# Performance work log

Hardware: AMD Instinct MI355X
Metric: run time of the kernel (lower is better)

Reference implementation:

```python
import jax, jax.numpy as jnp
import numpy as np

N_NODES = 100000
N_EDGES = 640000
D = 128
EPS = 1e-5

def _full_layer_norm(x):
    # torch layer_norm with normalized_shape == x.shape: stats over ALL elements
    mu = jnp.mean(x)
    var = jnp.mean(jnp.square(x - mu))  # biased variance
    return (x - mu) * jax.lax.rsqrt(var + EPS)

def setup_inputs() -> dict:
    key = jax.random.key(0)
    k1, k2, k3, k4, k5 = jax.random.split(key, 5)
    scale1 = 1.0 / np.sqrt(D)
    scale2 = 1.0 / np.sqrt(2 * D)
    return {
        "edge_features": jax.random.normal(k1, (N_EDGES, D), dtype=jnp.float32),
        "node_features": jax.random.normal(k2, (N_NODES, D), dtype=jnp.float32),
        "edge_indices": jax.random.randint(k3, (N_EDGES, 2), 0, N_NODES, dtype=jnp.int32),
        "W1": jax.random.normal(k4, (D, D), dtype=jnp.float32) * scale1,
        "b1": jnp.zeros((D,), dtype=jnp.float32),
        "W2": jax.random.normal(k5, (2 * D, D), dtype=jnp.float32) * scale2,
        "b2": jnp.zeros((D,), dtype=jnp.float32),
    }

def reference(edge_features, node_features, edge_indices, W1, b1, W2, b2):
    # node MLP: linear -> whole-tensor layernorm -> gelu
    h = node_features @ W1 + b1                       # [N, D]
    h = jax.nn.gelu(_full_layer_norm(h), approximate=False)
    # gather source-node features onto edges
    src = edge_indices[:, 0]
    dst = edge_indices[:, 1]
    gathered = h[src]                                 # [E, D]
    e = jnp.concatenate([edge_features, gathered], axis=1)  # [E, 2D]
    e = e @ W2 + b2                                   # [E, D]
    e = jax.nn.gelu(_full_layer_norm(e), approximate=False)
    # scatter-mean (include_self=False): nodes with no in-edges stay 0
    seg_sum = jax.ops.segment_sum(e, dst, num_segments=N_NODES)       # [N, D]
    counts = jax.ops.segment_sum(jnp.ones((e.shape[0],), e.dtype), dst,
                                 num_segments=N_NODES)                 # [N]
    counts = counts[:, None]
    return jnp.where(counts > 0, seg_sum / jnp.maximum(counts, 1.0), 0.0)
```

## Files before the change

kernel.cpp:

```cpp
#include <hip/hip_runtime.h>
#include <hip/hip_bf16.h>
#include <math.h>

typedef __bf16 bf16;
typedef bf16 bf16x8 __attribute__((ext_vector_type(8)));
typedef float f32x4 __attribute__((ext_vector_type(4)));
typedef unsigned short ushort_t;

#define N_NODES 100000
#define N_EDGES 640000
#define DD 128
#define MAXDEG 64

__device__ __forceinline__ float gelu_f(float x) {
    return 0.5f * x * (1.0f + erff(x * 0.70710678118654752440f));
}

__device__ __forceinline__ float gelu_fast(float x) {
    float z2 = x * (1.595769122f + 0.071354816f * x * x);
    return x * __builtin_amdgcn_rcpf(1.0f + __expf(-z2));
}

__device__ __forceinline__ ushort_t bf16_bits(float x) {
    bf16 h = (bf16)x;
    return __builtin_bit_cast(ushort_t, h);
}

__device__ __forceinline__ float bits_to_f(ushort_t u) {
    return __uint_as_float(((unsigned)u) << 16);
}

#define K1_TILES 1563
__global__ __launch_bounds__(256) void k1_gemm1(
    const float* __restrict__ nf, const float* __restrict__ W1,
    const float* __restrict__ b1, ushort_t* __restrict__ hpre,
    float* __restrict__ psum, float* __restrict__ psq, int nblocks)
{
    __shared__ bf16 Ash[64 * 136];
    __shared__ float red[256];
    const int tid = threadIdx.x;
    const int lane = tid & 63;
    const int w = tid >> 6;
    const int l15 = lane & 15, l4 = lane >> 4;

    bf16x8 bfrag[4][2];
    #pragma unroll
    for (int s = 0; s < 4; ++s)
        #pragma unroll
        for (int t = 0; t < 2; ++t) {
            int n = w * 32 + t * 16 + l15;
            #pragma unroll
            for (int j = 0; j < 8; ++j)
                bfrag[s][t][j] = (bf16)W1[(s * 32 + l4 * 8 + j) * DD + n];
        }
    float bias[2];
    bias[0] = b1[w * 32 + l15];
    bias[1] = b1[w * 32 + 16 + l15];

    float lsum = 0.f, lsq = 0.f;
    const int srow = tid >> 2;
    const int q = tid & 3;

    for (int tile = blockIdx.x; tile < K1_TILES; tile += nblocks) {
        const int rbase = tile * 64;
        {
            int grow = min(rbase + srow, N_NODES - 1);
            const float4* p = (const float4*)&nf[(size_t)grow * DD + q * 32];
            #pragma unroll
            for (int u = 0; u < 4; ++u) {
                float4 a = p[2 * u], b = p[2 * u + 1];
                ushort_t o[8] = {bf16_bits(a.x), bf16_bits(a.y), bf16_bits(a.z), bf16_bits(a.w),
                                 bf16_bits(b.x), bf16_bits(b.y), bf16_bits(b.z), bf16_bits(b.w)};
                *(uint4*)&Ash[srow * 136 + q * 32 + u * 8] = *(const uint4*)o;
            }
        }
        __syncthreads();
        f32x4 acc[4][2];
        #pragma unroll
        for (int r = 0; r < 4; ++r)
            #pragma unroll
            for (int t = 0; t < 2; ++t)
                acc[r][t] = (f32x4){0.f, 0.f, 0.f, 0.f};
        #pragma unroll
        for (int s = 0; s < 4; ++s)
            #pragma unroll
            for (int r = 0; r < 4; ++r) {
                bf16x8 a = *(const bf16x8*)&Ash[(r * 16 + l15) * 136 + s * 32 + l4 * 8];
                acc[r][0] = __builtin_amdgcn_mfma_f32_16x16x32_bf16(a, bfrag[s][0], acc[r][0], 0, 0, 0);
                acc[r][1] = __builtin_amdgcn_mfma_f32_16x16x32_bf16(a, bfrag[s][1], acc[r][1], 0, 0, 0);
            }
        __syncthreads();
        #pragma unroll
        for (int r = 0; r < 4; ++r)
            #pragma unroll
            for (int t = 0; t < 2; ++t) {
                int n = w * 32 + t * 16 + l15;
                #pragma unroll
                for (int j = 0; j < 4; ++j) {
                    int rr = rbase + r * 16 + l4 * 4 + j;
                    if (rr < N_NODES) {
                        float v = acc[r][t][j] + bias[t];
                        hpre[(size_t)rr * DD + n] = bf16_bits(v);
                        lsum += v; lsq += v * v;
                    }
                }
            }
    }
    red[tid] = lsum; __syncthreads();
    for (int s = 128; s > 0; s >>= 1) { if (tid < s) red[tid] += red[tid + s]; __syncthreads(); }
    if (tid == 0) psum[blockIdx.x] = red[0];
    __syncthreads();
    red[tid] = lsq; __syncthreads();
    for (int s = 128; s > 0; s >>= 1) { if (tid < s) red[tid] += red[tid + s]; __syncthreads(); }
    if (tid == 0) psq[blockIdx.x] = red[0];
}

__global__ void k_reduce(const float* __restrict__ psum, const float* __restrict__ psq,
                         int nb, double cntd, float* __restrict__ scal)
{
    __shared__ double rs_[256], rq_[256];
    int tid = threadIdx.x;
    double s = 0.0, q = 0.0;
    for (int i = tid; i < nb; i += 256) { s += psum[i]; q += psq[i]; }
    rs_[tid] = s; rq_[tid] = q; __syncthreads();
    for (int st = 128; st > 0; st >>= 1) {
        if (tid < st) { rs_[tid] += rs_[tid + st]; rq_[tid] += rq_[tid + st]; }
        __syncthreads();
    }
    if (tid == 0) {
        double mu = rs_[0] / cntd;
        double var = rq_[0] / cntd - mu * mu;
        scal[0] = (float)mu;
        scal[1] = (float)(1.0 / sqrt(var + 1e-5));
    }
}

__global__ __launch_bounds__(256) void k3_act(
    const ushort_t* __restrict__ hpre, const float* __restrict__ scal,
    ushort_t* __restrict__ hg)
{
    const float mu = scal[0], rs = scal[1];
    size_t i = (size_t)(blockIdx.x * 256 + threadIdx.x) * 8;
    uint4 v = *(const uint4*)(hpre + i);
    const ushort_t* in = (const ushort_t*)&v;
    ushort_t o[8];
    #pragma unroll
    for (int j = 0; j < 8; ++j)
        o[j] = bf16_bits(gelu_f((bits_to_f(in[j]) - mu) * rs));
    *(uint4*)(hg + i) = *(const uint4*)o;
}

__global__ __launch_bounds__(256) void k4_gemm2(
    const float* __restrict__ ef, const ushort_t* __restrict__ hg,
    const int* __restrict__ eidx, const float* __restrict__ W2,
    const float* __restrict__ b2, ushort_t* __restrict__ e0,
    float* __restrict__ psum, float* __restrict__ psq, int nblocks)
{
    __shared__ bf16 Ash[64 * 264];
    __shared__ float red[256];
    const int tid = threadIdx.x;
    const int lane = tid & 63;
    const int w = tid >> 6;
    const int l15 = lane & 15, l4 = lane >> 4;

    bf16x8 bfrag[8][2];
    #pragma unroll
    for (int s = 0; s < 8; ++s)
        #pragma unroll
        for (int t = 0; t < 2; ++t) {
            int n = w * 32 + t * 16 + l15;
            #pragma unroll
            for (int j = 0; j < 8; ++j)
                bfrag[s][t][j] = (bf16)W2[(s * 32 + l4 * 8 + j) * DD + n];
        }
    float bias[2];
    bias[0] = b2[w * 32 + l15];
    bias[1] = b2[w * 32 + 16 + l15];

    float lsum = 0.f, lsq = 0.f;
    const int srow = tid >> 2;
    const int q = tid & 3;

    for (int tile = blockIdx.x; tile < N_EDGES / 64; tile += nblocks) {
        const int ebase = tile * 64;
        {
            const float4* p = (const float4*)&ef[(size_t)(ebase + srow) * DD + q * 32];
            #pragma unroll
            for (int u = 0; u < 4; ++u) {
                float4 a = p[2 * u], b = p[2 * u + 1];
                ushort_t o[8] = {bf16_bits(a.x), bf16_bits(a.y), bf16_bits(a.z), bf16_bits(a.w),
                                 bf16_bits(b.x), bf16_bits(b.y), bf16_bits(b.z), bf16_bits(b.w)};
                *(uint4*)&Ash[srow * 264 + q * 32 + u * 8] = *(const uint4*)o;
            }
            int src = eidx[(size_t)(ebase + srow) * 2];
            const uint4* hp = (const uint4*)&hg[(size_t)src * DD + q * 32];
            uint4* hd = (uint4*)&Ash[srow * 264 + 128 + q * 32];
            #pragma unroll
            for (int u = 0; u < 4; ++u) hd[u] = hp[u];
        }
        __syncthreads();
        f32x4 acc[4][2];
        #pragma unroll
        for (int r = 0; r < 4; ++r)
            #pragma unroll
            for (int t = 0; t < 2; ++t)
                acc[r][t] = (f32x4){0.f, 0.f, 0.f, 0.f};
        #pragma unroll
        for (int s = 0; s < 8; ++s)
            #pragma unroll
            for (int r = 0; r < 4; ++r) {
                bf16x8 a = *(const bf16x8*)&Ash[(r * 16 + l15) * 264 + s * 32 + l4 * 8];
                acc[r][0] = __builtin_amdgcn_mfma_f32_16x16x32_bf16(a, bfrag[s][0], acc[r][0], 0, 0, 0);
                acc[r][1] = __builtin_amdgcn_mfma_f32_16x16x32_bf16(a, bfrag[s][1], acc[r][1], 0, 0, 0);
            }
        __syncthreads();
        #pragma unroll
        for (int r = 0; r < 4; ++r)
            #pragma unroll
            for (int t = 0; t < 2; ++t) {
                int n = w * 32 + t * 16 + l15;
                #pragma unroll
                for (int j = 0; j < 4; ++j) {
                    float v = acc[r][t][j] + bias[t];
                    lsum += v; lsq += v * v;
                    int rr = ebase + r * 16 + l4 * 4 + j;
                    e0[(size_t)rr * DD + n] = bf16_bits(v);
                }
            }
    }
    red[tid] = lsum; __syncthreads();
    for (int s = 128; s > 0; s >>= 1) { if (tid < s) red[tid] += red[tid + s]; __syncthreads(); }
    if (tid == 0) psum[blockIdx.x] = red[0];
    __syncthreads();
    red[tid] = lsq; __syncthreads();
    for (int s = 128; s > 0; s >>= 1) { if (tid < s) red[tid] += red[tid + s]; __syncthreads(); }
    if (tid == 0) psq[blockIdx.x] = red[0];
}

__global__ __launch_bounds__(256) void k7_fill(
    const int* __restrict__ eidx, int* __restrict__ cnt, int* __restrict__ slot)
{
    int e = blockIdx.x * 256 + threadIdx.x;
    if (e >= N_EDGES) return;
    int dst = eidx[(size_t)e * 2 + 1];
    int pos = atomicAdd(&cnt[dst], 1);
    if (pos < MAXDEG) slot[dst * MAXDEG + pos] = e;
}

__global__ __launch_bounds__(256) void k8_gather(
    const ushort_t* __restrict__ e0v, const int* __restrict__ slot,
    const int* __restrict__ cnt, const float* __restrict__ scal,
    float* __restrict__ out)
{
    const float mu = scal[0], rs = scal[1];
    int node = (int)((blockIdx.x * 256 + threadIdx.x) >> 6);
    int lane = threadIdx.x & 63;
    if (node >= N_NODES) return;
    int c = cnt[node];
    int m = min(c, MAXDEG);
    int myslot = (lane < m) ? slot[node * MAXDEG + lane] : 0;
    float a0 = 0.f, a1 = 0.f;
    const size_t off = (size_t)(lane * 2);
    int j = 0;
    for (; j + 4 <= m; j += 4) {
        int ea = __shfl(myslot, j);
        int eb = __shfl(myslot, j + 1);
        int ec = __shfl(myslot, j + 2);
        int ed = __shfl(myslot, j + 3);
        unsigned ua = *(const unsigned*)&e0v[(size_t)ea * DD + off];
        unsigned ub = *(const unsigned*)&e0v[(size_t)eb * DD + off];
        unsigned uc = *(const unsigned*)&e0v[(size_t)ec * DD + off];
        unsigned ud = *(const unsigned*)&e0v[(size_t)ed * DD + off];
        a0 += gelu_fast((__uint_as_float(ua << 16) - mu) * rs);
        a1 += gelu_fast((__uint_as_float(ua & 0xffff0000u) - mu) * rs);
        a0 += gelu_fast((__uint_as_float(ub << 16) - mu) * rs);
        a1 += gelu_fast((__uint_as_float(ub & 0xffff0000u) - mu) * rs);
        a0 += gelu_fast((__uint_as_float(uc << 16) - mu) * rs);
        a1 += gelu_fast((__uint_as_float(uc & 0xffff0000u) - mu) * rs);
        a0 += gelu_fast((__uint_as_float(ud << 16) - mu) * rs);
        a1 += gelu_fast((__uint_as_float(ud & 0xffff0000u) - mu) * rs);
    }
    for (; j < m; ++j) {
        int ea = __shfl(myslot, j);
        unsigned ua = *(const unsigned*)&e0v[(size_t)ea * DD + off];
        a0 += gelu_fast((__uint_as_float(ua << 16) - mu) * rs);
        a1 += gelu_fast((__uint_as_float(ua & 0xffff0000u) - mu) * rs);
    }
    float inv = c > 0 ? 1.0f / (float)c : 0.f;
    out[(size_t)node * DD + lane * 2] = a0 * inv;
    out[(size_t)node * DD + lane * 2 + 1] = a1 * inv;
}

extern "C" void kernel_launch(void* const* d_in, const int* in_sizes, int n_in,
                              void* d_out, int out_size, void* d_ws, size_t ws_size,
                              hipStream_t stream) {
    const float* ef  = (const float*)d_in[0];
    const float* nf  = (const float*)d_in[1];
    const int*   eix = (const int*)d_in[2];
    const float* W1  = (const float*)d_in[3];
    const float* b1  = (const float*)d_in[4];
    const float* W2  = (const float*)d_in[5];
    const float* b2  = (const float*)d_in[6];
    float* out = (float*)d_out;
    char* ws = (char*)d_ws;

    ushort_t* hpre = (ushort_t*)(ws + 0);
    ushort_t* hg   = (ushort_t*)(ws + 25600000);
    ushort_t* e0   = (ushort_t*)(ws + 51200000);
    int*      cnt  = (int*)(ws + 215040000);
    int*      slot = (int*)(ws + 215440000);
    float*    p1s  = (float*)(ws + 241040000);
    float*    p1q  = p1s + 2048;
    float*    p2s  = (float*)(ws + 241060000);
    float*    p2q  = p2s + 2560;
    float*    s1   = (float*)(ws + 241090000);
    float*    s2   = (float*)(ws + 241090128);

    hipMemsetAsync(cnt, 0, N_NODES * sizeof(int), stream);
    k1_gemm1<<<521, 256, 0, stream>>>(nf, W1, b1, hpre, p1s, p1q, 521);
    k_reduce<<<1, 256, 0, stream>>>(p1s, p1q, 521, (double)N_NODES * DD, s1);
    k3_act<<<6250, 256, 0, stream>>>(hpre, s1, hg);
    k4_gemm2<<<2500, 256, 0, stream>>>(ef, hg, eix, W2, b2, e0, p2s, p2q, 2500);
    k_reduce<<<1, 256, 0, stream>>>(p2s, p2q, 2500, (double)N_EDGES * DD, s2);
    k7_fill<<<2500, 256, 0, stream>>>(eix, cnt, slot);
    k8_gather<<<25000, 256, 0, stream>>>(e0, slot, cnt, s2, out);
}
```

Baseline: 286.4 us.

## Replace reduce kernels with fixed-point atomic stats and vectorize GEMM epilogue stores

Removes the two single-block reduce kernels by having each GEMM block atomically add its partial sum and sum-of-squares as 64-bit fixed-point integers. Consumers then decode mean and rstd inline. The MFMA operand order is swapped so each lane holds 4 contiguous columns of one row, which allows packed 8-byte bf16 stores and float4 bias loads. The node GELU switches from erf to a fast sigmoid-based approximation, and the final output uses float2 stores. Fixed-point quantization of the statistics and the approximate GELU add small numerical error, and the stats buffer is zeroed by extending the existing memset.

After: 335.8 us. +17.3%, slower.

```diff
diff --git a/kernel.cpp b/kernel.cpp
--- a/kernel.cpp
+++ b/kernel.cpp
@@ -6,15 +6,13 @@
 typedef bf16 bf16x8 __attribute__((ext_vector_type(8)));
 typedef float f32x4 __attribute__((ext_vector_type(4)));
 typedef unsigned short ushort_t;
+typedef unsigned long long u64;
 
 #define N_NODES 100000
 #define N_EDGES 640000
 #define DD 128
 #define MAXDEG 64
-
-__device__ __forceinline__ float gelu_f(float x) {
-    return 0.5f * x * (1.0f + erff(x * 0.70710678118654752440f));
-}
+#define STAT_SCALE 1048576.0
 
 __device__ __forceinline__ float gelu_fast(float x) {
     float z2 = x * (1.595769122f + 0.071354816f * x * x);
@@ -28,13 +26,40 @@
 
 __device__ __forceinline__ float bits_to_f(ushort_t u) {
     return __uint_as_float(((unsigned)u) << 16);
+}
+
+__device__ __forceinline__ long long to_fixed(double x) {
+    return (long long)(x * STAT_SCALE + (x >= 0.0 ? 0.5 : -0.5));
+}
+
+__device__ __forceinline__ void stats_atomic(float lsum, float lsq, float* red,
+                                             u64* dsum, u64* dsq) {
+    int tid = threadIdx.x;
+    red[tid] = lsum; __syncthreads();
+    for (int s = 128; s > 0; s >>= 1) { if (tid < s) red[tid] += red[tid + s]; __syncthreads(); }
+    float bs = red[0]; __syncthreads();
+    red[tid] = lsq; __syncthreads();
+    for (int s = 128; s > 0; s >>= 1) { if (tid < s) red[tid] += red[tid + s]; __syncthreads(); }
+    if (tid == 0) {
+        atomicAdd(dsum, (u64)to_fixed((double)bs));
+        atomicAdd(dsq,  (u64)to_fixed((double)red[0]));
+    }
+}
+
+__device__ __forceinline__ void stats_decode(const u64* stats, double cnt,
+                                             float* mu, float* rs) {
+    long long ss = (long long)stats[0], sq = (long long)stats[1];
+    double mu_d = ((double)ss / STAT_SCALE) / cnt;
+    double var  = ((double)sq / STAT_SCALE) / cnt - mu_d * mu_d;
+    *mu = (float)mu_d;
+    *rs = (float)(1.0 / sqrt(var + 1e-5));
 }
 
 #define K1_TILES 1563
 __global__ __launch_bounds__(256) void k1_gemm1(
     const float* __restrict__ nf, const float* __restrict__ W1,
     const float* __restrict__ b1, ushort_t* __restrict__ hpre,
-    float* __restrict__ psum, float* __restrict__ psq, int nblocks)
+    u64* __restrict__ stats, int nblocks)
 {
     __shared__ bf16 Ash[64 * 136];
     __shared__ float red[256];
@@ -53,9 +78,9 @@
             for (int j = 0; j < 8; ++j)
                 bfrag[s][t][j] = (bf16)W1[(s * 32 + l4 * 8 + j) * DD + n];
         }
-    float bias[2];
-    bias[0] = b1[w * 32 + l15];
-    bias[1] = b1[w * 32 + 16 + l15];
+    float4 bias4[2];
+    bias4[0] = *(const float4*)&b1[w * 32 + l4 * 4];
+    bias4[1] = *(const float4*)&b1[w * 32 + 16 + l4 * 4];
 
     float lsum = 0.f, lsq = 0.f;
     const int srow = tid >> 2;
@@ -86,67 +111,45 @@
             #pragma unroll
             for (int r = 0; r < 4; ++r) {
                 bf16x8 a = *(const bf16x8*)&Ash[(r * 16 + l15) * 136 + s * 32 + l4 * 8];
-                acc[r][0] = __builtin_amdgcn_mfma_f32_16x16x32_bf16(a, bfrag[s][0], acc[r][0], 0, 0, 0);
-                acc[r][1] = __builtin_amdgcn_mfma_f32_16x16x32_bf16(a, bfrag[s][1], acc[r][1], 0, 0, 0);
+                acc[r][0] = __builtin_amdgcn_mfma_f32_16x16x32_bf16(bfrag[s][0], a, acc[r][0], 0, 0, 0);
+                acc[r][1] = __builtin_amdgcn_mfma_f32_16x16x32_bf16(bfrag[s][1], a, acc[r][1], 0, 0, 0);
             }
         __syncthreads();
         #pragma unroll
-        for (int r = 0; r < 4; ++r)
-            #pragma unroll
-            for (int t = 0; t < 2; ++t) {
-                int n = w * 32 + t * 16 + l15;
+        for (int r = 0; r < 4; ++r) {
+            int row = rbase + r * 16 + l15;
+            if (row < N_NODES) {
                 #pragma unroll
-                for (int j = 0; j < 4; ++j) {
-                    int rr = rbase + r * 16 + l4 * 4 + j;
-                    if (rr < N_NODES) {
-                        float v = acc[r][t][j] + bias[t];
-                        hpre[(size_t)rr * DD + n] = bf16_bits(v);
+                for (int t = 0; t < 2; ++t) {
+                    int col = w * 32 + t * 16 + l4 * 4;
+                    ushort_t o[4];
+                    #pragma unroll
+                    for (int j = 0; j < 4; ++j) {
+                        float v = acc[r][t][j] + bias4[t][j];
                         lsum += v; lsq += v * v;
+                        o[j] = bf16_bits(v);
                     }
+                    *(uint2*)&hpre[(size_t)row * DD + col] = *(const uint2*)o;
                 }
             }
-    }
-    red[tid] = lsum; __syncthreads();
-    for (int s = 128; s > 0; s >>= 1) { if (tid < s) red[tid] += red[tid + s]; __syncthreads(); }
-    if (tid == 0) psum[blockIdx.x] = red[0];
-    __syncthreads();
-    red[tid] = lsq; __syncthreads();
-    for (int s = 128; s > 0; s >>= 1) { if (tid < s) red[tid] += red[tid + s]; __syncthreads(); }
-    if (tid == 0) psq[blockIdx.x] = red[0];
-}
-
-__global__ void k_reduce(const float* __restrict__ psum, const float* __restrict__ psq,
-                         int nb, double cntd, float* __restrict__ scal)
-{
-    __shared__ double rs_[256], rq_[256];
-    int tid = threadIdx.x;
-    double s = 0.0, q = 0.0;
-    for (int i = tid; i < nb; i += 256) { s += psum[i]; q += psq[i]; }
-    rs_[tid] = s; rq_[tid] = q; __syncthreads();
-    for (int st = 128; st > 0; st >>= 1) {
-        if (tid < st) { rs_[tid] += rs_[tid + st]; rq_[tid] += rq_[tid + st]; }
-        __syncthreads();
-    }
-    if (tid == 0) {
-        double mu = rs_[0] / cntd;
-        double var = rq_[0] / cntd - mu * mu;
-        scal[0] = (float)mu;
-        scal[1] = (float)(1.0 / sqrt(var + 1e-5));
-    }
+        }
+    }
+    stats_atomic(lsum, lsq, red, &stats[0], &stats[1]);
 }
 
 __global__ __launch_bounds__(256) void k3_act(
-    const ushort_t* __restrict__ hpre, const float* __restrict__ scal,
+    const ushort_t* __restrict__ hpre, const u64* __restrict__ stats,
     ushort_t* __restrict__ hg)
 {
-    const float mu = scal[0], rs = scal[1];
+    float mu, rs;
+    stats_decode(stats, (double)N_NODES * DD, &mu, &rs);
     size_t i = (size_t)(blockIdx.x * 256 + threadIdx.x) * 8;
     uint4 v = *(const uint4*)(hpre + i);
     const ushort_t* in = (const ushort_t*)&v;
     ushort_t o[8];
     #pragma unroll
     for (int j = 0; j < 8; ++j)
-        o[j] = bf16_bits(gelu_f((bits_to_f(in[j]) - mu) * rs));
+        o[j] = bf16_bits(gelu_fast((bits_to_f(in[j]) - mu) * rs));
     *(uint4*)(hg + i) = *(const uint4*)o;
 }
 
@@ -154,7 +157,7 @@
     const float* __restrict__ ef, const ushort_t* __restrict__ hg,
     const int* __restrict__ eidx, const float* __restrict__ W2,
     const float* __restrict__ b2, ushort_t* __restrict__ e0,
-    float* __restrict__ psum, float* __restrict__ psq, int nblocks)
+    u64* __restrict__ stats, int nblocks)
 {
     __shared__ bf16 Ash[64 * 264];
     __shared__ float red[256];
@@ -173,9 +176,9 @@
             for (int j = 0; j < 8; ++j)
                 bfrag[s][t][j] = (bf16)W2[(s * 32 + l4 * 8 + j) * DD + n];
         }
-    float bias[2];
-    bias[0] = b2[w * 32 + l15];
-    bias[1] = b2[w * 32 + 16 + l15];
+    float4 bias4[2];
+    bias4[0] = *(const float4*)&b2[w * 32 + l4 * 4];
+    bias4[1] = *(const float4*)&b2[w * 32 + 16 + l4 * 4];
 
     float lsum = 0.f, lsq = 0.f;
     const int srow = tid >> 2;
@@ -210,31 +213,28 @@
             #pragma unroll
             for (int r = 0; r < 4; ++r) {
                 bf16x8 a = *(const bf16x8*)&Ash[(r * 16 + l15) * 264 + s * 32 + l4 * 8];
-                acc[r][0] = __builtin_amdgcn_mfma_f32_16x16x32_bf16(a, bfrag[s][0], acc[r][0], 0, 0, 0);
-                acc[r][1] = __builtin_amdgcn_mfma_f32_16x16x32_bf16(a, bfrag[s][1], acc[r][1], 0, 0, 0);
+                acc[r][0] = __builtin_amdgcn_mfma_f32_16x16x32_bf16(bfrag[s][0], a, acc[r][0], 0, 0, 0);
+                acc[r][1] = __builtin_amdgcn_mfma_f32_16x16x32_bf16(bfrag[s][1], a, acc[r][1], 0, 0, 0);
             }
         __syncthreads();
         #pragma unroll
-        for (int r = 0; r < 4; ++r)
+        for (int r = 0; r < 4; ++r) {
+            int row = ebase + r * 16 + l15;
             #pragma unroll
             for (int t = 0; t < 2; ++t) {
-                int n = w * 32 + t * 16 + l15;
+                int col = w * 32 + t * 16 + l4 * 4;
+                ushort_t o[4];
                 #pragma unroll
                 for (int j = 0; j < 4; ++j) {
-                    float v = acc[r][t][j] + bias[t];
+                    float v = acc[r][t][j] + bias4[t][j];
                     lsum += v; lsq += v * v;
-                    int rr = ebase + r * 16 + l4 * 4 + j;
-                    e0[(size_t)rr * DD + n] = bf16_bits(v);
+                    o[j] = bf16_bits(v);
                 }
-            }
-    }
-    red[tid] = lsum; __syncthreads();
-    for (int s = 128; s > 0; s >>= 1) { if (tid < s) red[tid] += red[tid + s]; __syncthreads(); }
-    if (tid == 0) psum[blockIdx.x] = red[0];
-    __syncthreads();
-    red[tid] = lsq; __syncthreads();
-    for (int s = 128; s > 0; s >>= 1) { if (tid < s) red[tid] += red[tid + s]; __syncthreads(); }
-    if (tid == 0) psq[blockIdx.x] = red[0];
+                *(uint2*)&e0[(size_t)row * DD + col] = *(const uint2*)o;
+            }
+        }
+    }
+    stats_atomic(lsum, lsq, red, &stats[2], &stats[3]);
 }
 
 __global__ __launch_bounds__(256) void k7_fill(
@@ -249,10 +249,11 @@
 
 __global__ __launch_bounds__(256) void k8_gather(
     const ushort_t* __restrict__ e0v, const int* __restrict__ slot,
-    const int* __restrict__ cnt, const float* __restrict__ scal,
+    const int* __restrict__ cnt, const u64* __restrict__ stats,
     float* __restrict__ out)
 {
-    const float mu = scal[0], rs = scal[1];
+    float mu, rs;
+    stats_decode(stats + 2, (double)N_EDGES * DD, &mu, &rs);
     int node = (int)((blockIdx.x * 256 + threadIdx.x) >> 6);
     int lane = threadIdx.x & 63;
     if (node >= N_NODES) return;
@@ -287,8 +288,8 @@
         a1 += gelu_fast((__uint_as_float(ua & 0xffff0000u) - mu) * rs);
     }
     float inv = c > 0 ? 1.0f / (float)c : 0.f;
-    out[(size_t)node * DD + lane * 2] = a0 * inv;
-    out[(size_t)node * DD + lane * 2 + 1] = a1 * inv;
+    float2 res = {a0 * inv, a1 * inv};
+    *(float2*)&out[(size_t)node * DD + lane * 2] = res;
 }
 
 extern "C" void kernel_launch(void* const* d_in, const int* in_sizes, int n_in,
@@ -304,24 +305,17 @@
     float* out = (float*)d_out;
     char* ws = (char*)d_ws;
 
-    ushort_t* hpre = (ushort_t*)(ws + 0);
-    ushort_t* hg   = (ushort_t*)(ws + 25600000);
-    ushort_t* e0   = (ushort_t*)(ws + 51200000);
-    int*      cnt  = (int*)(ws + 215040000);
-    int*      slot = (int*)(ws + 215440000);
-    float*    p1s  = (float*)(ws + 241040000);
-    float*    p1q  = p1s + 2048;
-    float*    p2s  = (float*)(ws + 241060000);
-    float*    p2q  = p2s + 2560;
-    float*    s1   = (float*)(ws + 241090000);
-    float*    s2   = (float*)(ws + 241090128);
-
-    hipMemsetAsync(cnt, 0, N_NODES * sizeof(int), stream);
-    k1_gemm1<<<521, 256, 0, stream>>>(nf, W1, b1, hpre, p1s, p1q, 521);
-    k_reduce<<<1, 256, 0, stream>>>(p1s, p1q, 521, (double)N_NODES * DD, s1);
-    k3_act<<<6250, 256, 0, stream>>>(hpre, s1, hg);
-    k4_gemm2<<<2500, 256, 0, stream>>>(ef, hg, eix, W2, b2, e0, p2s, p2q, 2500);
-    k_reduce<<<1, 256, 0, stream>>>(p2s, p2q, 2500, (double)N_EDGES * DD, s2);
+    ushort_t* hpre  = (ushort_t*)(ws + 0);
+    ushort_t* hg    = (ushort_t*)(ws + 25600000);
+    ushort_t* e0    = (ushort_t*)(ws + 51200000);
+    int*      cnt   = (int*)(ws + 215040000);
+    u64*      stats = (u64*)(ws + 215440000);
+    int*      slot  = (int*)(ws + 215440064);
+
+    hipMemsetAsync(cnt, 0, 400000 + 64, stream);
+    k1_gemm1<<<521, 256, 0, stream>>>(nf, W1, b1, hpre, stats, 521);
+    k3_act<<<6250, 256, 0, stream>>>(hpre, stats, hg);
     k7_fill<<<2500, 256, 0, stream>>>(eix, cnt, slot);
-    k8_gather<<<25000, 256, 0, stream>>>(e0, slot, cnt, s2, out);
-}
+    k4_gemm2<<<2500, 256, 0, stream>>>(ef, hg, eix, W2, b2, e0, stats, 2500);
+    k8_gather<<<25000, 256, 0, stream>>>(e0, slot, cnt, stats, out);
+}
```
